# Optimization experiments

Measured on AMD Instinct MI355X. Metric: run time of the kernel, lower is better.

The kernel has to match this reference:

```python
import jax, jax.numpy as jnp
import numpy as np

C_S = 1024
C_Z = 128
H = 16
D = C_S // H  # 64
INF = 1000000.0
B, I, J = 1, 1024, 1024


def setup_inputs() -> dict:
    key = jax.random.key(0)
    ks = jax.random.split(key, 10)
    sc = 0.02
    return {
        "s": jax.random.normal(ks[0], (B, I, C_S), jnp.float32),
        "k_in": jax.random.normal(ks[1], (B, J, C_S), jnp.float32),
        "mask": jnp.ones((B, J), jnp.float32),
        "bias": jax.random.normal(ks[2], (B, I, J, C_Z), jnp.float32),
        "Wq": jax.random.normal(ks[3], (C_S, C_S), jnp.float32) * sc,
        "bq": jax.random.normal(ks[4], (C_S,), jnp.float32) * sc,
        "Wk": jax.random.normal(ks[5], (C_S, C_S), jnp.float32) * sc,
        "Wv": jax.random.normal(ks[6], (C_S, C_S), jnp.float32) * sc,
        "Wg": jax.random.normal(ks[7], (C_S, C_S), jnp.float32) * sc,
        "Wo": jax.random.normal(ks[8], (C_S, C_S), jnp.float32) * sc,
        "Wz": jax.random.normal(ks[9], (C_Z, H), jnp.float32) * sc,
        "multiplicity": 1,
    }


def reference(s, k_in, mask, bias, Wq, bq, Wk, Wv, Wg, Wo, Wz, multiplicity):
    b = s.shape[0]
    # QKV projections (torch Linear: x @ W.T + b)
    q = (s @ Wq.T + bq).reshape(b, -1, H, D)        # [b, i, h, d]
    k = (k_in @ Wk.T).reshape(b, -1, H, D)          # [b, j, h, d]
    v = (k_in @ Wv.T).reshape(b, -1, H, D)          # [b, j, h, d]

    # pair bias: proj_z = Linear(c_z -> h, no bias) + rearrange to [b, h, i, j]
    z = jnp.einsum("bijc,ch->bhij", bias, Wz)
    z = jnp.repeat(z, multiplicity, axis=0)
    z = z + (1.0 - mask[:, None, None, :]) * (-INF)  # mask over key dim j

    g = jax.nn.sigmoid(s @ Wg.T)                    # [b, i, c_s]

    # attention in fp32 (original uses autocast-disabled fp32 block)
    attn = jnp.einsum("bihd,bjhd->bhij", q.astype(jnp.float32), k.astype(jnp.float32))
    attn = attn / (D ** 0.5) + z.astype(jnp.float32)
    attn = jax.nn.softmax(attn, axis=-1)
    o = jnp.einsum("bhij,bjhd->bihd", attn, v.astype(jnp.float32)).astype(v.dtype)

    o = o.reshape(b, -1, C_S)
    return (g * o) @ Wo.T
```

## Files before the change

kernel.cpp:

```cpp
#include <hip/hip_runtime.h>

typedef unsigned short u16;
typedef unsigned int   u32;
typedef __attribute__((ext_vector_type(8))) short bf16x8;
typedef __attribute__((ext_vector_type(4))) float f32x4;

#define MFMA16(a, b, c) __builtin_amdgcn_mfma_f32_16x16x32_bf16((a), (b), (c), 0, 0, 0)

__device__ __forceinline__ float bfu(u16 x) { return __uint_as_float(((u32)x) << 16); }
__device__ __forceinline__ u16 f2bf(float f) {
    u32 u = __float_as_uint(f);
    u32 r = u + 0x7fffu + ((u >> 16) & 1u);
    return (u16)(r >> 16);
}
__device__ __forceinline__ u32 pk2(float a, float b) {
    return (u32)f2bf(a) | ((u32)f2bf(b) << 16);
}
__device__ __forceinline__ bf16x8 cvt8(float4 a, float4 b) {
    bf16x8 r;
    r[0] = (short)f2bf(a.x); r[1] = (short)f2bf(a.y);
    r[2] = (short)f2bf(a.z); r[3] = (short)f2bf(a.w);
    r[4] = (short)f2bf(b.x); r[5] = (short)f2bf(b.y);
    r[6] = (short)f2bf(b.z); r[7] = (short)f2bf(b.w);
    return r;
}
__device__ __forceinline__ void gl_lds16(const u16* g, u16* l) {
    __builtin_amdgcn_global_load_lds(
        (const __attribute__((address_space(1))) void*)g,
        (__attribute__((address_space(3))) void*)l, 16, 0, 0);
}

struct CvtArgs { const float* src[7]; u16* dst[7]; };

__global__ __launch_bounds__(256) void convert_bf16(CvtArgs a) {
    const int tsel = blockIdx.x >> 6;
    const int blk  = blockIdx.x & 63;
    const float* s = a.src[tsel];
    u16* d = a.dst[tsel];
    const int base = blk * 16384;
    #pragma unroll 4
    for (int it = 0; it < 16; ++it) {
        const int idx = base + (it * 256 + threadIdx.x) * 4;
        float4 v = *(const float4*)(s + idx);
        uint2 p;
        p.x = pk2(v.x, v.y);
        p.y = pk2(v.z, v.w);
        *(uint2*)(d + idx) = p;
    }
}

template<int EPI>
__global__ __launch_bounds__(256) void gemmW(
    const u16* __restrict__ Ab, const u16* __restrict__ W0, const u16* __restrict__ W1,
    const float* __restrict__ bqv, void* __restrict__ C0, void* __restrict__ C1)
{
    __shared__ u16 lA[64 * 64];
    __shared__ u16 lB[64 * 64];
    const int t = threadIdx.x, lane = t & 63, w = t >> 6;
    const int ln = lane & 15, q4 = lane >> 4;
    const int wm = (w & 1) * 32, wn = (w >> 1) * 32;
    const int m0 = blockIdx.y * 64, n0 = blockIdx.x * 64;

    const u16* Wp = (n0 < 1024) ? (W0 + (size_t)n0 * 1024)
                                : (W1 + (size_t)(n0 - 1024) * 1024);
    const int srow = t >> 3, scol = (t & 7) * 8;
    const u16* ga = Ab + (m0 + srow) * 1024 + scol;
    const u16* gb = Wp + srow * 1024 + scol;
    u16* la = lA + t * 8;
    u16* lb = lB + t * 8;

    f32x4 acc00 = {0,0,0,0}, acc01 = {0,0,0,0}, acc10 = {0,0,0,0}, acc11 = {0,0,0,0};

    for (int k0 = 0; k0 < 1024; k0 += 64) {
        gl_lds16(ga + k0,             la);
        gl_lds16(ga + k0 + 32 * 1024, la + 32 * 64);
        gl_lds16(gb + k0,             lb);
        gl_lds16(gb + k0 + 32 * 1024, lb + 32 * 64);
        __syncthreads();
        #pragma unroll
        for (int ks = 0; ks < 2; ++ks) {
            bf16x8 a0 = *(const bf16x8*)(lA + (wm +      ln) * 64 + ks * 32 + q4 * 8);
            bf16x8 a1 = *(const bf16x8*)(lA + (wm + 16 + ln) * 64 + ks * 32 + q4 * 8);
            bf16x8 b0 = *(const bf16x8*)(lB + (wn +      ln) * 64 + ks * 32 + q4 * 8);
            bf16x8 b1 = *(const bf16x8*)(lB + (wn + 16 + ln) * 64 + ks * 32 + q4 * 8);
            acc00 = MFMA16(a0, b0, acc00);
            acc01 = MFMA16(a0, b1, acc01);
            acc10 = MFMA16(a1, b0, acc10);
            acc11 = MFMA16(a1, b1, acc11);
        }
        __syncthreads();
    }

    #pragma unroll
    for (int tm = 0; tm < 2; ++tm) {
        #pragma unroll
        for (int tn = 0; tn < 2; ++tn) {
            const f32x4 a = (tm == 0) ? (tn == 0 ? acc00 : acc01)
                                      : (tn == 0 ? acc10 : acc11);
            #pragma unroll
            for (int r = 0; r < 4; ++r) {
                const int gm = m0 + wm + tm * 16 + q4 * 4 + r;
                const int gn = n0 + wn + tn * 16 + ln;
                float cv = a[r];
                if (EPI == 0) {
                    if (gn < 1024) ((u16*)C0)[gm * 1024 + gn] = f2bf(cv + bqv[gn]);
                    else ((u16*)C1)[gm * 1024 + gn - 1024] =
                             f2bf(1.0f / (1.0f + __expf(-cv)));
                } else if (EPI == 1) {
                    if (gn < 1024) ((u16*)C0)[gm * 1024 + gn] = f2bf(cv);
                    else ((u16*)C1)[(gn - 1024) * 1024 + gm] = f2bf(cv);
                } else {
                    ((float*)C0)[gm * 1024 + gn] = cv;
                }
            }
        }
    }
}

__global__ __launch_bounds__(256) void zproj(
    const float* __restrict__ bias, const float* __restrict__ Wz, u16* __restrict__ z)
{
    __shared__ float lz[16 * 516];
    const int t = threadIdx.x, lane = t & 63, w = t >> 6;
    const int ln = lane & 15, q4 = lane >> 4;
    const int row0 = blockIdx.x * 512;

    bf16x8 bfrag[4];
    #pragma unroll
    for (int kb = 0; kb < 4; ++kb)
        #pragma unroll
        for (int j = 0; j < 8; ++j)
            bfrag[kb][j] = (short)f2bf(Wz[(kb * 32 + q4 * 8 + j) * 16 + ln]);

    #pragma unroll 1
    for (int it = 0; it < 8; ++it) {
        const int rloc = (it * 4 + w) * 16;
        const float* ap = bias + (size_t)(row0 + rloc + ln) * 128 + q4 * 8;
        f32x4 c = {0, 0, 0, 0};
        #pragma unroll
        for (int kb = 0; kb < 4; ++kb) {
            float4 x0 = *(const float4*)(ap + kb * 32);
            float4 x1 = *(const float4*)(ap + kb * 32 + 4);
            bf16x8 a = cvt8(x0, x1);
            c = MFMA16(a, bfrag[kb], c);
        }
        #pragma unroll
        for (int r = 0; r < 4; ++r)
            lz[ln * 516 + rloc + q4 * 4 + r] = c[r];
    }
    __syncthreads();
    #pragma unroll 4
    for (int rep = 0; rep < 32; ++rep) {
        const int idx = rep * 256 + t;
        const int hh = idx >> 9, r = idx & 511;
        z[(size_t)hh * 1048576 + row0 + r] = f2bf(lz[hh * 516 + r]);
    }
}

__global__ __launch_bounds__(256) void attn_kernel(
    const u16* __restrict__ qb, const u16* __restrict__ kmat,
    const u16* __restrict__ vT, const u16* __restrict__ zb,
    const float* __restrict__ maskb, const u16* __restrict__ gmat,
    u16* __restrict__ o)
{
    __shared__ u16 pbf[16 * 1032];
    __shared__ float redm[4][16];
    __shared__ float reds[4][16];
    const int h = blockIdx.y;
    const int i0 = blockIdx.x * 16;
    const int t = threadIdx.x, lane = t & 63, w = t >> 6;
    const int ln = lane & 15, q4 = lane >> 4;

    const u16* qp = qb + (i0 + ln) * 1024 + h * 64 + q4 * 8;
    const bf16x8 aq0 = *(const bf16x8*)(qp);
    const bf16x8 aq1 = *(const bf16x8*)(qp + 32);

    f32x4 s[16];
    #pragma unroll
    for (int u = 0; u < 16; ++u) {
        const int j0 = (w * 16 + u) * 16;
        const u16* kp = kmat + (j0 + ln) * 1024 + h * 64 + q4 * 8;
        bf16x8 b0 = *(const bf16x8*)(kp);
        bf16x8 b1 = *(const bf16x8*)(kp + 32);
        f32x4 c = {0, 0, 0, 0};
        c = MFMA16(aq0, b0, c);
        c = MFMA16(aq1, b1, c);
        const int j = j0 + ln;
        const float mt = (1.0f - maskb[j]) * (-1000000.0f);
        #pragma unroll
        for (int r = 0; r < 4; ++r) {
            const int gi = i0 + q4 * 4 + r;
            c[r] = c[r] * 0.125f + bfu(zb[(size_t)h * 1048576 + gi * 1024 + j]) + mt;
        }
        s[u] = c;
    }

    float mx[4];
    #pragma unroll
    for (int r = 0; r < 4; ++r) {
        float m_ = s[0][r];
        #pragma unroll
        for (int u = 1; u < 16; ++u) m_ = fmaxf(m_, s[u][r]);
        #pragma unroll
        for (int off = 1; off < 16; off <<= 1) m_ = fmaxf(m_, __shfl_xor(m_, off));
        mx[r] = m_;
    }
    if (ln == 0) {
        #pragma unroll
        for (int r = 0; r < 4; ++r) redm[w][q4 * 4 + r] = mx[r];
    }
    __syncthreads();

    float inv[4];
    #pragma unroll
    for (int r = 0; r < 4; ++r) {
        const int row = q4 * 4 + r;
        const float m_ = fmaxf(fmaxf(redm[0][row], redm[1][row]),
                               fmaxf(redm[2][row], redm[3][row]));
        float s_ = 0.f;
        #pragma unroll
        for (int u = 0; u < 16; ++u) {
            float e = __expf(s[u][r] - m_);
            s[u][r] = e;
            s_ += e;
        }
        #pragma unroll
        for (int off = 1; off < 16; off <<= 1) s_ += __shfl_xor(s_, off);
        mx[r] = s_;
    }
    if (ln == 0) {
        #pragma unroll
        for (int r = 0; r < 4; ++r) reds[w][q4 * 4 + r] = mx[r];
    }
    __syncthreads();
    #pragma unroll
    for (int r = 0; r < 4; ++r) {
        const int row = q4 * 4 + r;
        inv[r] = 1.0f / (reds[0][row] + reds[1][row] + reds[2][row] + reds[3][row]);
    }

    #pragma unroll
    for (int u = 0; u < 16; ++u) {
        const int j0 = (w * 16 + u) * 16;
        #pragma unroll
        for (int r = 0; r < 4; ++r)
            pbf[(q4 * 4 + r) * 1032 + j0 + ln] = f2bf(s[u][r] * inv[r]);
    }
    __syncthreads();

    f32x4 oc = {0, 0, 0, 0};
    #pragma unroll 4
    for (int ks = 0; ks < 32; ++ks) {
        bf16x8 pa = *(const bf16x8*)(pbf + ln * 1032 + ks * 32 + q4 * 8);
        bf16x8 vb = *(const bf16x8*)(vT + (h * 64 + w * 16 + ln) * 1024 + ks * 32 + q4 * 8);
        oc = MFMA16(pa, vb, oc);
    }
    const int col = h * 64 + w * 16 + ln;
    #pragma unroll
    for (int r = 0; r < 4; ++r) {
        const int gi = i0 + q4 * 4 + r;
        const float gv = bfu(gmat[gi * 1024 + col]);
        o[gi * 1024 + col] = f2bf(oc[r] * gv);
    }
}

extern "C" void kernel_launch(void* const* d_in, const int* in_sizes, int n_in,
                              void* d_out, int out_size, void* d_ws, size_t ws_size,
                              hipStream_t stream)
{
    const float* s_in = (const float*)d_in[0];
    const float* k_in = (const float*)d_in[1];
    const float* mask = (const float*)d_in[2];
    const float* bias = (const float*)d_in[3];
    const float* Wq   = (const float*)d_in[4];
    const float* bq   = (const float*)d_in[5];
    const float* Wk   = (const float*)d_in[6];
    const float* Wv   = (const float*)d_in[7];
    const float* Wg   = (const float*)d_in[8];
    const float* Wo   = (const float*)d_in[9];
    const float* Wz   = (const float*)d_in[10];

    char* ws = (char*)d_ws;
    const size_t MB = 1 << 20;
    u16* sb  = (u16*)(ws + 0 * MB);
    u16* kbf = (u16*)(ws + 2 * MB);
    u16* Wqb = (u16*)(ws + 4 * MB);
    u16* Wkb = (u16*)(ws + 6 * MB);
    u16* Wvb = (u16*)(ws + 8 * MB);
    u16* Wgb = (u16*)(ws + 10 * MB);
    u16* Wob = (u16*)(ws + 12 * MB);
    u16* q   = (u16*)(ws + 14 * MB);
    u16* kk  = (u16*)(ws + 16 * MB);
    u16* vT  = (u16*)(ws + 18 * MB);
    u16* g   = (u16*)(ws + 20 * MB);
    u16* og  = (u16*)(ws + 22 * MB);
    u16* z   = (u16*)(ws + 24 * MB);
    float* out = (float*)d_out;

    CvtArgs ca;
    ca.src[0] = s_in; ca.dst[0] = sb;
    ca.src[1] = k_in; ca.dst[1] = kbf;
    ca.src[2] = Wq;   ca.dst[2] = Wqb;
    ca.src[3] = Wk;   ca.dst[3] = Wkb;
    ca.src[4] = Wv;   ca.dst[4] = Wvb;
    ca.src[5] = Wg;   ca.dst[5] = Wgb;
    ca.src[6] = Wo;   ca.dst[6] = Wob;

    const dim3 blk(256);
    hipLaunchKernelGGL(convert_bf16, dim3(448), blk, 0, stream, ca);
    hipLaunchKernelGGL(gemmW<0>, dim3(32, 16), blk, 0, stream, sb,  Wqb, Wgb, bq, q,  g);
    hipLaunchKernelGGL(gemmW<1>, dim3(32, 16), blk, 0, stream, kbf, Wkb, Wvb, nullptr, kk, vT);
    hipLaunchKernelGGL(zproj, dim3(2048), blk, 0, stream, bias, Wz, z);
    hipLaunchKernelGGL(attn_kernel, dim3(64, 16), blk, 0, stream, q, kk, vT, z, mask, g, og);
    hipLaunchKernelGGL(gemmW<2>, dim3(16, 16), blk, 0, stream, og, Wob, nullptr, nullptr, out, nullptr);
}
```

Before: 814.3 us.

## Merge launches and split-K the output projection for better occupancy

Folds the bf16 conversion into the z-projection kernel as extra blocks and merges the two QKVG GEMM launches into one grid with a z dimension. This cuts launch count and lets independent work share the GPU. The output projection was a 256-block grid, so it is now split along K into four partial fp32 buffers and summed by a separate reduce kernel. That fills more CUs but adds 16MB of partial-buffer traffic and an extra launch.

```diff
diff --git a/kernel.cpp b/kernel.cpp
--- a/kernel.cpp
+++ b/kernel.cpp
@@ -32,30 +32,82 @@
 
 struct CvtArgs { const float* src[7]; u16* dst[7]; };
 
-__global__ __launch_bounds__(256) void convert_bf16(CvtArgs a) {
-    const int tsel = blockIdx.x >> 6;
-    const int blk  = blockIdx.x & 63;
-    const float* s = a.src[tsel];
-    u16* d = a.dst[tsel];
-    const int base = blk * 16384;
+__global__ __launch_bounds__(256) void zproj_cvt(
+    const float* __restrict__ bias, const float* __restrict__ Wz,
+    u16* __restrict__ z, CvtArgs ca)
+{
+    __shared__ float lz[16 * 516];
+    const int t = threadIdx.x;
+
+    if (blockIdx.x >= 2048) {
+        const int blk  = blockIdx.x - 2048;
+        const int tsel = blk >> 6;
+        const float* s = ca.src[tsel];
+        u16* d = ca.dst[tsel];
+        const int base = (blk & 63) * 16384;
+        #pragma unroll 4
+        for (int it = 0; it < 16; ++it) {
+            const int idx = base + (it * 256 + t) * 4;
+            float4 v = *(const float4*)(s + idx);
+            uint2 p;
+            p.x = pk2(v.x, v.y);
+            p.y = pk2(v.z, v.w);
+            *(uint2*)(d + idx) = p;
+        }
+        return;
+    }
+
+    const int lane = t & 63, w = t >> 6;
+    const int ln = lane & 15, q4 = lane >> 4;
+    const int row0 = blockIdx.x * 512;
+
+    bf16x8 bfrag[4];
+    #pragma unroll
+    for (int kb = 0; kb < 4; ++kb)
+        #pragma unroll
+        for (int j = 0; j < 8; ++j)
+            bfrag[kb][j] = (short)f2bf(Wz[(kb * 32 + q4 * 8 + j) * 16 + ln]);
+
+    #pragma unroll 1
+    for (int it = 0; it < 8; ++it) {
+        const int rloc = (it * 4 + w) * 16;
+        const float* ap = bias + (size_t)(row0 + rloc + ln) * 128 + q4 * 8;
+        f32x4 c = {0, 0, 0, 0};
+        #pragma unroll
+        for (int kb = 0; kb < 4; ++kb) {
+            float4 x0 = *(const float4*)(ap + kb * 32);
+            float4 x1 = *(const float4*)(ap + kb * 32 + 4);
+            bf16x8 a = cvt8(x0, x1);
+            c = MFMA16(a, bfrag[kb], c);
+        }
+        #pragma unroll
+        for (int r = 0; r < 4; ++r)
+            lz[ln * 516 + rloc + q4 * 4 + r] = c[r];
+    }
+    __syncthreads();
     #pragma unroll 4
-    for (int it = 0; it < 16; ++it) {
-        const int idx = base + (it * 256 + threadIdx.x) * 4;
-        float4 v = *(const float4*)(s + idx);
-        uint2 p;
-        p.x = pk2(v.x, v.y);
-        p.y = pk2(v.z, v.w);
-        *(uint2*)(d + idx) = p;
-    }
-}
-
-template<int EPI>
-__global__ __launch_bounds__(256) void gemmW(
-    const u16* __restrict__ Ab, const u16* __restrict__ W0, const u16* __restrict__ W1,
-    const float* __restrict__ bqv, void* __restrict__ C0, void* __restrict__ C1)
+    for (int rep = 0; rep < 32; ++rep) {
+        const int idx = rep * 256 + t;
+        const int hh = idx >> 9, r = idx & 511;
+        z[(size_t)hh * 1048576 + row0 + r] = f2bf(lz[hh * 516 + r]);
+    }
+}
+
+__global__ __launch_bounds__(256) void gemm_qkvg(
+    const u16* __restrict__ sb, const u16* __restrict__ kbf,
+    const u16* __restrict__ Wqb, const u16* __restrict__ Wgb,
+    const u16* __restrict__ Wkb, const u16* __restrict__ Wvb,
+    const float* __restrict__ bqv,
+    u16* __restrict__ q, u16* __restrict__ g,
+    u16* __restrict__ kk, u16* __restrict__ vT)
 {
     __shared__ u16 lA[64 * 64];
     __shared__ u16 lB[64 * 64];
+    const int zb = blockIdx.z;
+    const u16* Ab = zb ? kbf : sb;
+    const u16* W0 = zb ? Wkb : Wqb;
+    const u16* W1 = zb ? Wvb : Wgb;
+
     const int t = threadIdx.x, lane = t & 63, w = t >> 6;
     const int ln = lane & 15, q4 = lane >> 4;
     const int wm = (w & 1) * 32, wn = (w >> 1) * 32;
@@ -102,58 +154,15 @@
                 const int gm = m0 + wm + tm * 16 + q4 * 4 + r;
                 const int gn = n0 + wn + tn * 16 + ln;
                 float cv = a[r];
-                if (EPI == 0) {
-                    if (gn < 1024) ((u16*)C0)[gm * 1024 + gn] = f2bf(cv + bqv[gn]);
-                    else ((u16*)C1)[gm * 1024 + gn - 1024] =
-                             f2bf(1.0f / (1.0f + __expf(-cv)));
-                } else if (EPI == 1) {
-                    if (gn < 1024) ((u16*)C0)[gm * 1024 + gn] = f2bf(cv);
-                    else ((u16*)C1)[(gn - 1024) * 1024 + gm] = f2bf(cv);
+                if (zb == 0) {
+                    if (gn < 1024) q[gm * 1024 + gn] = f2bf(cv + bqv[gn]);
+                    else g[gm * 1024 + gn - 1024] = f2bf(1.0f / (1.0f + __expf(-cv)));
                 } else {
-                    ((float*)C0)[gm * 1024 + gn] = cv;
+                    if (gn < 1024) kk[gm * 1024 + gn] = f2bf(cv);
+                    else vT[(gn - 1024) * 1024 + gm] = f2bf(cv);
                 }
             }
         }
-    }
-}
-
-__global__ __launch_bounds__(256) void zproj(
-    const float* __restrict__ bias, const float* __restrict__ Wz, u16* __restrict__ z)
-{
-    __shared__ float lz[16 * 516];
-    const int t = threadIdx.x, lane = t & 63, w = t >> 6;
-    const int ln = lane & 15, q4 = lane >> 4;
-    const int row0 = blockIdx.x * 512;
-
-    bf16x8 bfrag[4];
-    #pragma unroll
-    for (int kb = 0; kb < 4; ++kb)
-        #pragma unroll
-        for (int j = 0; j < 8; ++j)
-            bfrag[kb][j] = (short)f2bf(Wz[(kb * 32 + q4 * 8 + j) * 16 + ln]);
-
-    #pragma unroll 1
-    for (int it = 0; it < 8; ++it) {
-        const int rloc = (it * 4 + w) * 16;
-        const float* ap = bias + (size_t)(row0 + rloc + ln) * 128 + q4 * 8;
-        f32x4 c = {0, 0, 0, 0};
-        #pragma unroll
-        for (int kb = 0; kb < 4; ++kb) {
-            float4 x0 = *(const float4*)(ap + kb * 32);
-            float4 x1 = *(const float4*)(ap + kb * 32 + 4);
-            bf16x8 a = cvt8(x0, x1);
-            c = MFMA16(a, bfrag[kb], c);
-        }
-        #pragma unroll
-        for (int r = 0; r < 4; ++r)
-            lz[ln * 516 + rloc + q4 * 4 + r] = c[r];
-    }
-    __syncthreads();
-    #pragma unroll 4
-    for (int rep = 0; rep < 32; ++rep) {
-        const int idx = rep * 256 + t;
-        const int hh = idx >> 9, r = idx & 511;
-        z[(size_t)hh * 1048576 + row0 + r] = f2bf(lz[hh * 516 + r]);
     }
 }
 
@@ -262,6 +271,78 @@
         const float gv = bfu(gmat[gi * 1024 + col]);
         o[gi * 1024 + col] = f2bf(oc[r] * gv);
     }
+}
+
+__global__ __launch_bounds__(256) void gemm_out_sk(
+    const u16* __restrict__ og, const u16* __restrict__ Wob, float* __restrict__ pbuf)
+{
+    __shared__ u16 lA[64 * 64];
+    __shared__ u16 lB[64 * 64];
+    const int t = threadIdx.x, lane = t & 63, w = t >> 6;
+    const int ln = lane & 15, q4 = lane >> 4;
+    const int wm = (w & 1) * 32, wn = (w >> 1) * 32;
+    const int m0 = blockIdx.y * 64, n0 = blockIdx.x * 64;
+    const int kz = blockIdx.z;
+
+    const int srow = t >> 3, scol = (t & 7) * 8;
+    const u16* ga = og  + (m0 + srow) * 1024 + scol + kz * 256;
+    const u16* gb = Wob + (n0 + srow) * 1024 + scol + kz * 256;
+    u16* la = lA + t * 8;
+    u16* lb = lB + t * 8;
+
+    f32x4 acc00 = {0,0,0,0}, acc01 = {0,0,0,0}, acc10 = {0,0,0,0}, acc11 = {0,0,0,0};
+
+    for (int k0 = 0; k0 < 256; k0 += 64) {
+        gl_lds16(ga + k0,             la);
+        gl_lds16(ga + k0 + 32 * 1024, la + 32 * 64);
+        gl_lds16(gb + k0,             lb);
+        gl_lds16(gb + k0 + 32 * 1024, lb + 32 * 64);
+        __syncthreads();
+        #pragma unroll
+        for (int ks = 0; ks < 2; ++ks) {
+            bf16x8 a0 = *(const bf16x8*)(lA + (wm +      ln) * 64 + ks * 32 + q4 * 8);
+            bf16x8 a1 = *(const bf16x8*)(lA + (wm + 16 + ln) * 64 + ks * 32 + q4 * 8);
+            bf16x8 b0 = *(const bf16x8*)(lB + (wn +      ln) * 64 + ks * 32 + q4 * 8);
+            bf16x8 b1 = *(const bf16x8*)(lB + (wn + 16 + ln) * 64 + ks * 32 + q4 * 8);
+            acc00 = MFMA16(a0, b0, acc00);
+            acc01 = MFMA16(a0, b1, acc01);
+            acc10 = MFMA16(a1, b0, acc10);
+            acc11 = MFMA16(a1, b1, acc11);
+        }
+        __syncthreads();
+    }
+
+    float* pz = pbuf + (size_t)kz * 1048576;
+    #pragma unroll
+    for (int tm = 0; tm < 2; ++tm) {
+        #pragma unroll
+        for (int tn = 0; tn < 2; ++tn) {
+            const f32x4 a = (tm == 0) ? (tn == 0 ? acc00 : acc01)
+                                      : (tn == 0 ? acc10 : acc11);
+            #pragma unroll
+            for (int r = 0; r < 4; ++r) {
+                const int gm = m0 + wm + tm * 16 + q4 * 4 + r;
+                const int gn = n0 + wn + tn * 16 + ln;
+                pz[gm * 1024 + gn] = a[r];
+            }
+        }
+    }
+}
+
+__global__ __launch_bounds__(256) void reduce4(
+    const float* __restrict__ p, float* __restrict__ out)
+{
+    const int idx = (blockIdx.x * 256 + threadIdx.x) * 4;
+    float4 a = *(const float4*)(p + idx);
+    float4 b = *(const float4*)(p + 1048576 + idx);
+    float4 c = *(const float4*)(p + 2097152 + idx);
+    float4 d = *(const float4*)(p + 3145728 + idx);
+    float4 r;
+    r.x = (a.x + b.x) + (c.x + d.x);
+    r.y = (a.y + b.y) + (c.y + d.y);
+    r.z = (a.z + b.z) + (c.z + d.z);
+    r.w = (a.w + b.w) + (c.w + d.w);
+    *(float4*)(out + idx) = r;
 }
 
 extern "C" void kernel_launch(void* const* d_in, const int* in_sizes, int n_in,
@@ -295,6 +376,7 @@
     u16* g   = (u16*)(ws + 20 * MB);
     u16* og  = (u16*)(ws + 22 * MB);
     u16* z   = (u16*)(ws + 24 * MB);
+    float* pbuf = (float*)(ws + 56 * MB);
     float* out = (float*)d_out;
 
     CvtArgs ca;
@@ -307,10 +389,11 @@
     ca.src[6] = Wo;   ca.dst[6] = Wob;
 
     const dim3 blk(256);
-    hipLaunchKernelGGL(convert_bf16, dim3(448), blk, 0, stream, ca);
-    hipLaunchKernelGGL(gemmW<0>, dim3(32, 16), blk, 0, stream, sb,  Wqb, Wgb, bq, q,  g);
-    hipLaunchKernelGGL(gemmW<1>, dim3(32, 16), blk, 0, stream, kbf, Wkb, Wvb, nullptr, kk, vT);
-    hipLaunchKernelGGL(zproj, dim3(2048), blk, 0, stream, bias, Wz, z);
-    hipLaunchKernelGGL(attn_kernel, dim3(64, 16), blk, 0, stream, q, kk, vT, z, mask, g, og);
-    hipLaunchKernelGGL(gemmW<2>, dim3(16, 16), blk, 0, stream, og, Wob, nullptr, nullptr, out, nullptr);
-}
+    hipLaunchKernelGGL(zproj_cvt, dim3(2496), blk, 0, stream, bias, Wz, z, ca);
+    hipLaunchKernelGGL(gemm_qkvg, dim3(32, 16, 2), blk, 0, stream,
+                       sb, kbf, Wqb, Wgb, Wkb, Wvb, bq, q, g, kk, vT);
+    hipLaunchKernelGGL(attn_kernel, dim3(64, 16), blk, 0, stream,
+                       q, kk, vT, z, mask, g, og);
+    hipLaunchKernelGGL(gemm_out_sk, dim3(16, 16, 4), blk, 0, stream, og, Wob, pbuf);
+    hipLaunchKernelGGL(reduce4, dim3(1024), blk, 0, stream, pbuf, out);
+}
```

New measurement: 801.4 us. Within noise of the previous version (-1.6%).
